# Optimization experiments

Hardware: AMD Instinct MI355X
Metric: run time of the kernel (lower is better)

The kernel has to match this reference:

```python
import jax, jax.numpy as jnp
import numpy as np

D_MODEL = 1024
NUM_HEADS = 16
HEAD_DIM = D_MODEL // NUM_HEADS
BATCH = 8
SEQ = 2048
LN_EPS = 1e-5


def setup_inputs() -> dict:
    rng = jax.random.key(0)
    ks = jax.random.split(rng, 16)
    s = 0.02  # init scale for weights
    w = lambda k: jax.random.normal(k, (D_MODEL, D_MODEL), jnp.float32) * s
    return {
        "query": jax.random.normal(ks[0], (BATCH, SEQ, D_MODEL), jnp.float32),
        "key": jax.random.normal(ks[1], (BATCH, SEQ, D_MODEL), jnp.float32),
        "value": jax.random.normal(ks[2], (BATCH, SEQ, D_MODEL), jnp.float32),
        "Wq": w(ks[3]), "bq": jnp.zeros((D_MODEL,), jnp.float32),
        "Wk": w(ks[4]), "bk": jnp.zeros((D_MODEL,), jnp.float32),
        "Wv": w(ks[5]), "bv": jnp.zeros((D_MODEL,), jnp.float32),
        "ln_g": jnp.ones((D_MODEL,), jnp.float32),
        "ln_b": jnp.zeros((D_MODEL,), jnp.float32),
        "Wo": w(ks[6]), "bo": jnp.zeros((D_MODEL,), jnp.float32),
    }


def reference(query, key, value, Wq, bq, Wk, bk, Wv, bv, ln_g, ln_b, Wo, bo):
    N, L, dm = query.shape
    H, Dh = NUM_HEADS, HEAD_DIM
    # projections + split heads -> (N, H, L, Dh), matching torch .view().transpose(1,2)
    q = (query @ Wq.T + bq).reshape(N, L, H, Dh).transpose(0, 2, 1, 3)
    k = (key   @ Wk.T + bk).reshape(N, L, H, Dh).transpose(0, 2, 1, 3)
    v = (value @ Wv.T + bv).reshape(N, L, H, Dh).transpose(0, 2, 1, 3)
    # Faithful to source: einsum 'nqhd,nkhd->nhqk' applied to ALREADY-transposed
    # (N,H,L,Dh) tensors => per-position head-to-head attention, energy (N, L, H, H).
    energy = jnp.einsum('nhld,ngld->nlhg', q, k)  # (N, L, H, H)
    attn = jax.nn.softmax(energy / jnp.sqrt(jnp.float32(dm)), axis=3)
    # source einsum 'nhql,nlhd->nqhd' on transposed v -> (N, H, L, Dh)
    out = jnp.einsum('nlhg,ngld->nhld', attn, v)
    out = out.transpose(0, 2, 1, 3).reshape(N, L, dm)
    # dropout is identity in eval mode
    mu = out.mean(axis=-1, keepdims=True)
    var = out.var(axis=-1, keepdims=True)
    out = (out - mu) / jnp.sqrt(var + LN_EPS) * ln_g + ln_b
    return out @ Wo.T + bo
```

## Files before the change

kernel.cpp:

```cpp
#include <hip/hip_runtime.h>
#include <cstdint>

#define TOKENS 16384
#define DMODEL 1024
#define NHEADS 16
#define HDIM   64

typedef __bf16  bf16x8 __attribute__((ext_vector_type(8)));
typedef ushort  u16x8  __attribute__((ext_vector_type(8)));
typedef ushort  u16x4  __attribute__((ext_vector_type(4)));
typedef short   s16x4  __attribute__((ext_vector_type(4)));
typedef float   f32x4  __attribute__((ext_vector_type(4)));

#if defined(__has_builtin)
#if __has_builtin(__builtin_amdgcn_mfma_f32_16x16x16bf16_1k)
#define HAVE_MFMA_K16 1
#endif
#endif

__device__ __forceinline__ ushort f2bf(float f) {
    union { float f; unsigned int i; } v; v.f = f;
    return (ushort)((v.i + 0x8000u) >> 16);
}
__device__ __forceinline__ f32x4 mfma16(bf16x8 a, bf16x8 b, f32x4 c) {
    return __builtin_amdgcn_mfma_f32_16x16x32_bf16(a, b, c, 0, 0, 0);
}
__device__ __forceinline__ void gload_lds16(const void* g, void* l) {
    __builtin_amdgcn_global_load_lds(
        (const __attribute__((address_space(1))) unsigned int*)(uintptr_t)g,
        (__attribute__((address_space(3))) unsigned int*)(uintptr_t)l,
        16, 0, 0);
}
union BU { u16x8 u; bf16x8 b; };

struct CvtArgs {
    const float* src[4];
    ushort*      dst[4];
};

__global__ __launch_bounds__(256) void cvt_f32_bf16(CvtArgs a)
{
    const float* __restrict__ s = a.src[blockIdx.y];
    ushort*      __restrict__ d = a.dst[blockIdx.y];
    const long i = ((long)blockIdx.x * 256 + threadIdx.x) * 8;
    const f32x4 v0 = *(const f32x4*)(s + i);
    const f32x4 v1 = *(const f32x4*)(s + i + 4);
    u16x8 p;
    #pragma unroll
    for (int j = 0; j < 4; j++) {
        p[j]     = f2bf(v0[j]);
        p[4 + j] = f2bf(v1[j]);
    }
    *(u16x8*)(d + i) = p;
}

#define BM2 256
#define BN2 256
#define BK2 32

struct GemmArgs {
    const ushort* A[3];
    const ushort* W[3];
    const float*  Bi[3];
    void*         C[3];
};

#define G256_READ_B(slot)                                                     \
    { _Pragma("unroll")                                                       \
      for (int n = 0; n < 4; ++n)                                             \
          bf[n] = *(const bf16x8*)&Bs[slot][(wn * 64 + n * 16 + fr) * BK2 + fks]; }

#define G256_READ_A(slot, mh)                                                 \
    { _Pragma("unroll")                                                       \
      for (int m = 0; m < 4; ++m)                                             \
          af[m] = *(const bf16x8*)&As[slot][(wm * 128 + (mh) * 64 + m * 16 + fr) * BK2 + fks]; }

#define G256_MFMA(mh)                                                         \
    { __builtin_amdgcn_s_setprio(1);                                          \
      _Pragma("unroll")                                                       \
      for (int m = 0; m < 4; ++m)                                             \
          _Pragma("unroll")                                                   \
          for (int n = 0; n < 4; ++n)                                         \
              acc[(mh) * 4 + m][n] = mfma16(af[m], bf[n], acc[(mh) * 4 + m][n]); \
      __builtin_amdgcn_s_setprio(0); }

template<int BF16OUT>
__global__ __launch_bounds__(512) void gemm256(GemmArgs args, int N, int K)
{
    __shared__ __align__(16) ushort As[4][BM2 * BK2];
    __shared__ __align__(16) ushort Bs[4][BN2 * BK2];

    const int gx = gridDim.x, gy = gridDim.y;
    const int lin = (blockIdx.z * gy + blockIdx.y) * gx + blockIdx.x;
    const int nwg = gx * gy * gridDim.z;
    const int q = nwg >> 3, r = nwg & 7;
    const int xcd = lin & 7, loc = lin >> 3;
    const int swz = (xcd < r ? xcd * (q + 1) : r * (q + 1) + (xcd - r) * q) + loc;
    const int bz  = swz / (gx * gy);
    const int rem = swz - bz * gx * gy;
    const int by  = rem / gx;
    const int bx  = rem - by * gx;

    const ushort* __restrict__ A  = args.A[bz];
    const ushort* __restrict__ W  = args.W[bz];
    const float*  __restrict__ Bi = args.Bi[bz];

    const int tid  = threadIdx.x;
    const int wave = tid >> 6;
    const int lane = tid & 63;
    const int wm = wave >> 2;
    const int wn = wave & 3;
    const long rowBase = (long)by * BM2;
    const long colBase = (long)bx * BN2;

    const int gA0 = tid, gA1 = tid + 512;
    const long aOff0 = (long)(gA0 >> 2) * K + (((gA0 & 3) ^ ((gA0 >> 3) & 3)) * 8);
    const long aOff1 = (long)(gA1 >> 2) * K + (((gA1 & 3) ^ ((gA1 >> 3) & 3)) * 8);
    const ushort* Abase = A + rowBase * K;
    const ushort* Wbase = W + colBase * K;

    const int fr  = lane & 15;
    const int fks = (((lane >> 4) ^ ((fr >> 1) & 3)) * 8);

    f32x4 acc[8][4];
    #pragma unroll
    for (int m = 0; m < 8; ++m)
        #pragma unroll
        for (int n = 0; n < 4; ++n)
            acc[m][n] = (f32x4){0.f, 0.f, 0.f, 0.f};

    auto stageA = [&](int slot, int kt) {
        gload_lds16(Abase + aOff0 + (long)kt * BK2, &As[slot][gA0 * 8]);
        gload_lds16(Abase + aOff1 + (long)kt * BK2, &As[slot][gA1 * 8]);
    };
    auto stageB = [&](int slot, int kt) {
        gload_lds16(Wbase + aOff0 + (long)kt * BK2, &Bs[slot][gA0 * 8]);
        gload_lds16(Wbase + aOff1 + (long)kt * BK2, &Bs[slot][gA1 * 8]);
    };

    const int nt = K / BK2;

    stageA(0, 0); stageB(0, 0);
    stageA(1, 1); stageB(1, 1);
    stageA(2, 2); stageB(2, 2);
    asm volatile("s_waitcnt vmcnt(8)" ::: "memory");
    __builtin_amdgcn_s_barrier();

    bf16x8 af[4], bf[4];

    for (int X = 0; X < nt - 3; ++X) {
        const int slot = X & 3, st = (X + 3) & 3;
        G256_READ_B(slot);
        G256_READ_A(slot, 0);
        stageA(st, X + 3);
        G256_MFMA(0);
        __builtin_amdgcn_s_barrier();
        G256_READ_A(slot, 1);
        stageB(st, X + 3);
        G256_MFMA(1);
        asm volatile("s_waitcnt vmcnt(8)" ::: "memory");
        __builtin_amdgcn_s_barrier();
    }
    {
        const int slot = (nt - 3) & 3;
        G256_READ_B(slot);
        G256_READ_A(slot, 0);
        G256_MFMA(0);
        __builtin_amdgcn_s_barrier();
        G256_READ_A(slot, 1);
        G256_MFMA(1);
        asm volatile("s_waitcnt vmcnt(4)" ::: "memory");
        __builtin_amdgcn_s_barrier();
    }
    {
        const int slot = (nt - 2) & 3;
        G256_READ_B(slot);
        G256_READ_A(slot, 0);
        G256_MFMA(0);
        __builtin_amdgcn_s_barrier();
        G256_READ_A(slot, 1);
        G256_MFMA(1);
        asm volatile("s_waitcnt vmcnt(0)" ::: "memory");
        __builtin_amdgcn_s_barrier();
    }
    {
        const int slot = (nt - 1) & 3;
        G256_READ_B(slot);
        G256_READ_A(slot, 0);
        G256_MFMA(0);
        __builtin_amdgcn_s_barrier();
        G256_READ_A(slot, 1);
        G256_MFMA(1);
    }

    const int qd = lane >> 4;
    #pragma unroll
    for (int n = 0; n < 4; ++n) {
        const long col = colBase + wn * 64 + n * 16 + fr;
        const float bv = Bi[col];
        #pragma unroll
        for (int m = 0; m < 8; ++m) {
            const long r0 = rowBase + wm * 128 + m * 16 + qd * 4;
            #pragma unroll
            for (int r2 = 0; r2 < 4; ++r2) {
                const float val = acc[m][n][r2] + bv;
                if (BF16OUT)
                    ((ushort*)args.C[bz])[(r0 + r2) * (long)N + col] = f2bf(val);
                else
                    ((float*)args.C[bz])[(r0 + r2) * (long)N + col] = val;
            }
        }
    }
}

#define PMS 40

__global__ __launch_bounds__(256) void attn_ln_mfma(
    const ushort* __restrict__ Qp, const ushort* __restrict__ Kp,
    const ushort* __restrict__ Vp,
    const float* __restrict__ lng, const float* __restrict__ lnb,
    ushort* __restrict__ O)
{
#if HAVE_MFMA_K16
    __shared__ __align__(16) ushort Vs[4][1024];
#else
    __shared__ __align__(16) ushort Vs[4][2048];
    __shared__ __align__(16) ushort Pm[4][16 * PMS];
#endif
    __shared__ __align__(16) float Os[4][16 * 68];

    const int tid  = threadIdx.x;
    const int w    = tid >> 6;
    const int lane = tid & 63;
    const long tok  = (long)blockIdx.x * 4 + w;
    const long base = tok * DMODEL;

    {
        const int i0 = lane, i1 = lane + 64;
        const int g0 = i0 >> 3, d80 = (i0 & 7) ^ (((i0 >> 5) & 3) << 1);
        const int g1 = i1 >> 3, d81 = (i1 & 7) ^ (((i1 >> 5) & 3) << 1);
        gload_lds16(Vp + base + g0 * 64 + d80 * 8, &Vs[w][i0 * 8]);
        gload_lds16(Vp + base + g1 * 64 + d81 * 8, &Vs[w][i1 * 8]);
    }

    const int fr = lane & 15;
    const int hi = lane >> 4;
    const int fs = hi * 8;

    const bf16x8 aq0 = *(const bf16x8*)(Qp + base + fr * 64 + fs);
    const bf16x8 aq1 = *(const bf16x8*)(Qp + base + fr * 64 + fs + 32);
    const bf16x8 bk0 = *(const bf16x8*)(Kp + base + fr * 64 + fs);
    const bf16x8 bk1 = *(const bf16x8*)(Kp + base + fr * 64 + fs + 32);

    f32x4 e = (f32x4){0.f, 0.f, 0.f, 0.f};
    e = mfma16(bk0, aq0, e);
    e = mfma16(bk1, aq1, e);

    float x[4];
    #pragma unroll
    for (int r = 0; r < 4; ++r) x[r] = e[r] * 0.03125f;
    float mx = fmaxf(fmaxf(x[0], x[1]), fmaxf(x[2], x[3]));
    mx = fmaxf(mx, __shfl_xor(mx, 16, 64));
    mx = fmaxf(mx, __shfl_xor(mx, 32, 64));
    float ex[4], sm;
    #pragma unroll
    for (int r = 0; r < 4; ++r) ex[r] = __expf(x[r] - mx);
    sm = (ex[0] + ex[1]) + (ex[2] + ex[3]);
    sm += __shfl_xor(sm, 16, 64);
    sm += __shfl_xor(sm, 32, 64);
    const float inv = 1.0f / sm;
    float p[4];
    #pragma unroll
    for (int r = 0; r < 4; ++r) p[r] = ex[r] * inv;

    f32x4 o[4];

#if HAVE_MFMA_K16
    s16x4 pa;
    #pragma unroll
    for (int r = 0; r < 4; ++r) pa[r] = (short)f2bf(p[r]);

    asm volatile("s_waitcnt vmcnt(0)" ::: "memory");

    #pragma unroll
    for (int dblk = 0; dblk < 4; ++dblk) {
        s16x4 bv;
        #pragma unroll
        for (int j = 0; j < 4; ++j) {
            const int g = hi * 4 + j;
            const int d = dblk * 16 + fr;
            const int ad = g * 64 + (((d >> 3) ^ (((g >> 2) & 3) << 1)) * 8) + (d & 7);
            bv[j] = (short)Vs[w][ad];
        }
        o[dblk] = __builtin_amdgcn_mfma_f32_16x16x16bf16_1k(
            pa, bv, (f32x4){0.f, 0.f, 0.f, 0.f}, 0, 0, 0);
    }
#else
    *(u16x4*)&Pm[w][fr * PMS + 16 + hi * 4] = (u16x4){0, 0, 0, 0};
    #pragma unroll
    for (int r = 0; r < 4; ++r)
        Pm[w][fr * PMS + hi * 4 + r] = f2bf(p[r]);
    asm volatile("s_waitcnt vmcnt(0)" ::: "memory");
    const bf16x8 pa8 = *(const bf16x8*)&Pm[w][fr * PMS + fs];
    #pragma unroll
    for (int dblk = 0; dblk < 4; ++dblk) {
        BU bu;
        #pragma unroll
        for (int j = 0; j < 8; ++j) {
            const int g = fs + j;
            const int d = dblk * 16 + fr;
            const int ad = g * 64 + (((d >> 3) ^ (((g >> 2) & 3) << 1)) * 8) + (d & 7);
            bu.u[j] = Vs[w][ad];
        }
        o[dblk] = mfma16(pa8, bu.b, (f32x4){0.f, 0.f, 0.f, 0.f});
    }
#endif

    float s1 = 0.f, s2 = 0.f;
    #pragma unroll
    for (int dblk = 0; dblk < 4; ++dblk)
        #pragma unroll
        for (int r = 0; r < 4; ++r) { const float v = o[dblk][r]; s1 += v; s2 += v * v; }
    #pragma unroll
    for (int m = 1; m < 64; m <<= 1) {
        s1 += __shfl_xor(s1, m, 64);
        s2 += __shfl_xor(s2, m, 64);
    }
    const float mu   = s1 * (1.f / DMODEL);
    const float var  = s2 * (1.f / DMODEL) - mu * mu;
    const float rstd = rsqrtf(var + 1e-5f);

    #pragma unroll
    for (int dblk = 0; dblk < 4; ++dblk)
        #pragma unroll
        for (int r = 0; r < 4; ++r)
            Os[w][(hi * 4 + r) * 68 + dblk * 16 + fr] = (o[dblk][r] - mu) * rstd;

    u16x8 s0, s1v;
    #pragma unroll
    for (int c = 0; c < 4; ++c) {
        const f32x4 yv = *(const f32x4*)&Os[w][(lane >> 2) * 68 + (lane & 3) * 16 + c * 4];
        const f32x4 lg = *(const f32x4*)(lng + lane * 16 + c * 4);
        const f32x4 lb = *(const f32x4*)(lnb + lane * 16 + c * 4);
        #pragma unroll
        for (int j = 0; j < 4; ++j) {
            const ushort hv = f2bf(yv[j] * lg[j] + lb[j]);
            if (c < 2) s0[c * 4 + j] = hv; else s1v[(c - 2) * 4 + j] = hv;
        }
    }
    *(u16x8*)(O + base + lane * 16)     = s0;
    *(u16x8*)(O + base + lane * 16 + 8) = s1v;
}

extern "C" void kernel_launch(void* const* d_in, const int* in_sizes, int n_in,
                              void* d_out, int out_size, void* d_ws, size_t ws_size,
                              hipStream_t stream)
{
    const float* query = (const float*)d_in[0];
    const float* key   = (const float*)d_in[1];
    const float* value = (const float*)d_in[2];
    const float* Wq = (const float*)d_in[3];
    const float* bq = (const float*)d_in[4];
    const float* Wk = (const float*)d_in[5];
    const float* bk = (const float*)d_in[6];
    const float* Wv = (const float*)d_in[7];
    const float* bv = (const float*)d_in[8];
    const float* lng = (const float*)d_in[9];
    const float* lnb = (const float*)d_in[10];
    const float* Wo = (const float*)d_in[11];
    const float* bo = (const float*)d_in[12];
    float* out = (float*)d_out;

    const long WELEMS = (long)DMODEL * DMODEL;

    ushort* wq_b = (ushort*)d_ws;
    ushort* wk_b = wq_b + WELEMS;
    ushort* wv_b = wk_b + WELEMS;
    ushort* wo_b = wv_b + WELEMS;
    ushort* cbuf = wo_b + WELEMS;

    int NC = 1;
    while (NC < 64 &&
           (size_t)(8 * WELEMS) + (size_t)(TOKENS / NC) * DMODEL * 10 > ws_size)
        NC <<= 1;
    const int CM = TOKENS / NC;
    const size_t CE = (size_t)CM * DMODEL;

    ushort* qb = cbuf;
    ushort* kb = qb + CE;
    ushort* vb = kb + CE;
    ushort* qp = vb + CE;
    ushort* vp = qp + CE;

    {
        CvtArgs cw;
        cw.src[0] = Wq; cw.src[1] = Wk; cw.src[2] = Wv; cw.src[3] = Wo;
        cw.dst[0] = wq_b; cw.dst[1] = wk_b; cw.dst[2] = wv_b; cw.dst[3] = wo_b;
        cvt_f32_bf16<<<dim3((unsigned)(WELEMS / 2048), 4), 256, 0, stream>>>(cw);
    }

    for (int c = 0; c < NC; ++c) {
        const size_t off = (size_t)c * CE;
        ushort* kp = (ushort*)(out + off);

        {
            CvtArgs ci;
            ci.src[0] = query + off; ci.src[1] = key + off; ci.src[2] = value + off;
            ci.src[3] = query;
            ci.dst[0] = qb; ci.dst[1] = kb; ci.dst[2] = vb; ci.dst[3] = qb;
            cvt_f32_bf16<<<dim3((unsigned)(CE / 2048), 3), 256, 0, stream>>>(ci);
        }

        GemmArgs g1;
        g1.A[0] = qb;    g1.A[1] = kb;   g1.A[2] = vb;
        g1.W[0] = wq_b;  g1.W[1] = wk_b; g1.W[2] = wv_b;
        g1.Bi[0] = bq;   g1.Bi[1] = bk;  g1.Bi[2] = bv;
        g1.C[0] = qp;    g1.C[1] = kp;   g1.C[2] = vp;
        gemm256<1><<<dim3(DMODEL / BN2, CM / BM2, 3), 512, 0, stream>>>(
            g1, DMODEL, DMODEL);

        attn_ln_mfma<<<CM / 4, 256, 0, stream>>>(qp, kp, vp, lng, lnb, qb);

        GemmArgs g2;
        g2.A[0] = g2.A[1] = g2.A[2] = qb;
        g2.W[0] = g2.W[1] = g2.W[2] = wo_b;
        g2.Bi[0] = g2.Bi[1] = g2.Bi[2] = bo;
        g2.C[0] = g2.C[1] = g2.C[2] = out + off;
        gemm256<0><<<dim3(DMODEL / BN2, CM / BM2, 1), 512, 0, stream>>>(
            g2, DMODEL, DMODEL);
    }
}
```

Measured before the change: 433.6 us.

## Fuse fp32-to-bf16 input conversion into QKV projection GEMM A-tile staging

The QKV GEMM now reads fp32 activations directly from global memory into registers, converts them to bf16 and writes them into swizzled LDS slots. A new register double-buffered pipeline replaces the async direct-to-LDS loads for A, which removes the separate conversion kernel and its bf16 round trip through memory. Attention now writes its output in place over the Q buffer, so the workspace needs fewer chunk buffers and fewer chunks may be used. The trade-offs are more register pressure, reading twice the A bytes inside the GEMM, and a more complex waitcnt schedule.

```diff
diff --git a/kernel.cpp b/kernel.cpp
--- a/kernel.cpp
+++ b/kernel.cpp
@@ -59,7 +59,7 @@
 #define BK2 32
 
 struct GemmArgs {
-    const ushort* A[3];
+    const void*   A[3];
     const ushort* W[3];
     const float*  Bi[3];
     void*         C[3];
@@ -84,7 +84,41 @@
               acc[(mh) * 4 + m][n] = mfma16(af[m], bf[n], acc[(mh) * 4 + m][n]); \
       __builtin_amdgcn_s_setprio(0); }
 
-template<int BF16OUT>
+#define ISSUE_A(P, kt)                                                        \
+    {   const float* ap_ = Af + (kt);                                         \
+        P##0 = *(const f32x4*)(ap_ + aF0);                                    \
+        P##1 = *(const f32x4*)(ap_ + aF0 + 4);                                \
+        P##2 = *(const f32x4*)(ap_ + aF1);                                    \
+        P##3 = *(const f32x4*)(ap_ + aF1 + 4);                                \
+    }
+#define WRITE_A(slot, P)                                                      \
+    {   u16x8 p0_, p1_;                                                       \
+        _Pragma("unroll")                                                     \
+        for (int j_ = 0; j_ < 4; ++j_) {                                      \
+            p0_[j_] = f2bf(P##0[j_]); p0_[4 + j_] = f2bf(P##1[j_]);           \
+            p1_[j_] = f2bf(P##2[j_]); p1_[4 + j_] = f2bf(P##3[j_]);           \
+        }                                                                     \
+        *(u16x8*)&As[slot][wg0 * 8] = p0_;                                    \
+        *(u16x8*)&As[slot][wg1 * 8] = p1_;                                    \
+    }
+
+#define STEADY_TILE(XV, IB, WB)                                               \
+    {   const int slot_ = (XV) & 3, st_ = ((XV) + 3) & 3;                     \
+        G256_READ_B(slot_);                                                   \
+        G256_READ_A(slot_, 0);                                                \
+        ISSUE_A(IB, ((XV) + 2) * BK2);                                        \
+        G256_MFMA(0);                                                         \
+        __builtin_amdgcn_s_barrier();                                         \
+        G256_READ_A(slot_, 1);                                                \
+        stageB(st_, (XV) + 3);                                                \
+        asm volatile("s_waitcnt vmcnt(8)" ::: "memory");                      \
+        WRITE_A(((XV) + 1) & 3, WB);                                          \
+        G256_MFMA(1);                                                         \
+        asm volatile("s_waitcnt lgkmcnt(0)" ::: "memory");                    \
+        __builtin_amdgcn_s_barrier();                                         \
+    }
+
+template<int BF16OUT, int AFP32>
 __global__ __launch_bounds__(512) void gemm256(GemmArgs args, int N, int K)
 {
     __shared__ __align__(16) ushort As[4][BM2 * BK2];
@@ -101,7 +135,6 @@
     const int by  = rem / gx;
     const int bx  = rem - by * gx;
 
-    const ushort* __restrict__ A  = args.A[bz];
     const ushort* __restrict__ W  = args.W[bz];
     const float*  __restrict__ Bi = args.Bi[bz];
 
@@ -114,10 +147,16 @@
     const long colBase = (long)bx * BN2;
 
     const int gA0 = tid, gA1 = tid + 512;
-    const long aOff0 = (long)(gA0 >> 2) * K + (((gA0 & 3) ^ ((gA0 >> 3) & 3)) * 8);
-    const long aOff1 = (long)(gA1 >> 2) * K + (((gA1 & 3) ^ ((gA1 >> 3) & 3)) * 8);
-    const ushort* Abase = A + rowBase * K;
+    const long sOff0 = (long)(gA0 >> 2) * K + (((gA0 & 3) ^ ((gA0 >> 3) & 3)) * 8);
+    const long sOff1 = (long)(gA1 >> 2) * K + (((gA1 & 3) ^ ((gA1 >> 3) & 3)) * 8);
     const ushort* Wbase = W + colBase * K;
+
+    const int arow0 = gA0 >> 2, arow1 = gA1 >> 2;
+    const long aF0 = (long)arow0 * K + (gA0 & 3) * 8;
+    const long aF1 = (long)arow1 * K + (gA1 & 3) * 8;
+    const int wg0 = arow0 * 4 + ((gA0 & 3) ^ ((arow0 >> 1) & 3));
+    const int wg1 = arow1 * 4 + ((gA1 & 3) ^ ((arow1 >> 1) & 3));
+    const float* Af = (const float*)args.A[bz] + rowBase * K;
 
     const int fr  = lane & 15;
     const int fks = (((lane >> 4) ^ ((fr >> 1) & 3)) * 8);
@@ -129,68 +168,126 @@
         for (int n = 0; n < 4; ++n)
             acc[m][n] = (f32x4){0.f, 0.f, 0.f, 0.f};
 
-    auto stageA = [&](int slot, int kt) {
-        gload_lds16(Abase + aOff0 + (long)kt * BK2, &As[slot][gA0 * 8]);
-        gload_lds16(Abase + aOff1 + (long)kt * BK2, &As[slot][gA1 * 8]);
+    auto stageB = [&](int slot, int kt) {
+        gload_lds16(Wbase + sOff0 + (long)kt * BK2, &Bs[slot][gA0 * 8]);
+        gload_lds16(Wbase + sOff1 + (long)kt * BK2, &Bs[slot][gA1 * 8]);
     };
-    auto stageB = [&](int slot, int kt) {
-        gload_lds16(Wbase + aOff0 + (long)kt * BK2, &Bs[slot][gA0 * 8]);
-        gload_lds16(Wbase + aOff1 + (long)kt * BK2, &Bs[slot][gA1 * 8]);
-    };
 
     const int nt = K / BK2;
-
-    stageA(0, 0); stageB(0, 0);
-    stageA(1, 1); stageB(1, 1);
-    stageA(2, 2); stageB(2, 2);
-    asm volatile("s_waitcnt vmcnt(8)" ::: "memory");
-    __builtin_amdgcn_s_barrier();
-
     bf16x8 af[4], bf[4];
 
-    for (int X = 0; X < nt - 3; ++X) {
-        const int slot = X & 3, st = (X + 3) & 3;
-        G256_READ_B(slot);
-        G256_READ_A(slot, 0);
-        stageA(st, X + 3);
-        G256_MFMA(0);
+    if constexpr (AFP32) {
+        f32x4 arA0, arA1, arA2, arA3, arB0, arB1, arB2, arB3;
+
+        ISSUE_A(arA, 0);
+        ISSUE_A(arB, BK2);
+        stageB(0, 0); stageB(1, 1); stageB(2, 2);
+        asm volatile("s_waitcnt vmcnt(10)" ::: "memory");
+        WRITE_A(0, arA);
+        asm volatile("s_waitcnt vmcnt(4)" ::: "memory");
+        asm volatile("s_waitcnt lgkmcnt(0)" ::: "memory");
         __builtin_amdgcn_s_barrier();
-        G256_READ_A(slot, 1);
-        stageB(st, X + 3);
-        G256_MFMA(1);
+
+        int X = 0;
+        for (; X + 1 <= nt - 5; X += 2) {
+            STEADY_TILE(X,     arA, arB);
+            STEADY_TILE(X + 1, arB, arA);
+        }
+        STEADY_TILE(nt - 4, arA, arB);
+
+        {
+            const int slot_ = (nt - 3) & 3;
+            G256_READ_B(slot_);
+            G256_READ_A(slot_, 0);
+            ISSUE_A(arB, (nt - 1) * BK2);
+            G256_MFMA(0);
+            __builtin_amdgcn_s_barrier();
+            G256_READ_A(slot_, 1);
+            asm volatile("s_waitcnt vmcnt(6)" ::: "memory");
+            WRITE_A((nt - 2) & 3, arA);
+            G256_MFMA(1);
+            asm volatile("s_waitcnt lgkmcnt(0)" ::: "memory");
+            __builtin_amdgcn_s_barrier();
+        }
+        {
+            const int slot_ = (nt - 2) & 3;
+            G256_READ_B(slot_);
+            G256_READ_A(slot_, 0);
+            G256_MFMA(0);
+            __builtin_amdgcn_s_barrier();
+            G256_READ_A(slot_, 1);
+            asm volatile("s_waitcnt vmcnt(0)" ::: "memory");
+            WRITE_A((nt - 1) & 3, arB);
+            G256_MFMA(1);
+            asm volatile("s_waitcnt lgkmcnt(0)" ::: "memory");
+            __builtin_amdgcn_s_barrier();
+        }
+        {
+            const int slot_ = (nt - 1) & 3;
+            G256_READ_B(slot_);
+            G256_READ_A(slot_, 0);
+            G256_MFMA(0);
+            __builtin_amdgcn_s_barrier();
+            G256_READ_A(slot_, 1);
+            G256_MFMA(1);
+        }
+    } else {
+        const ushort* Abase = (const ushort*)args.A[bz] + rowBase * K;
+        auto stageA = [&](int slot, int kt) {
+            gload_lds16(Abase + sOff0 + (long)kt * BK2, &As[slot][gA0 * 8]);
+            gload_lds16(Abase + sOff1 + (long)kt * BK2, &As[slot][gA1 * 8]);
+        };
+
+        stageA(0, 0); stageB(0, 0);
+        stageA(1, 1); stageB(1, 1);
+        stageA(2, 2); stageB(2, 2);
         asm volatile("s_waitcnt vmcnt(8)" ::: "memory");
         __builtin_amdgcn_s_barrier();
-    }
-    {
-        const int slot = (nt - 3) & 3;
-        G256_READ_B(slot);
-        G256_READ_A(slot, 0);
-        G256_MFMA(0);
-        __builtin_amdgcn_s_barrier();
-        G256_READ_A(slot, 1);
-        G256_MFMA(1);
-        asm volatile("s_waitcnt vmcnt(4)" ::: "memory");
-        __builtin_amdgcn_s_barrier();
-    }
-    {
-        const int slot = (nt - 2) & 3;
-        G256_READ_B(slot);
-        G256_READ_A(slot, 0);
-        G256_MFMA(0);
-        __builtin_amdgcn_s_barrier();
-        G256_READ_A(slot, 1);
-        G256_MFMA(1);
-        asm volatile("s_waitcnt vmcnt(0)" ::: "memory");
-        __builtin_amdgcn_s_barrier();
-    }
-    {
-        const int slot = (nt - 1) & 3;
-        G256_READ_B(slot);
-        G256_READ_A(slot, 0);
-        G256_MFMA(0);
-        __builtin_amdgcn_s_barrier();
-        G256_READ_A(slot, 1);
-        G256_MFMA(1);
+
+        for (int X = 0; X < nt - 3; ++X) {
+            const int slot_ = X & 3, st_ = (X + 3) & 3;
+            G256_READ_B(slot_);
+            G256_READ_A(slot_, 0);
+            stageA(st_, X + 3);
+            G256_MFMA(0);
+            __builtin_amdgcn_s_barrier();
+            G256_READ_A(slot_, 1);
+            stageB(st_, X + 3);
+            G256_MFMA(1);
+            asm volatile("s_waitcnt vmcnt(8)" ::: "memory");
+            __builtin_amdgcn_s_barrier();
+        }
+        {
+            const int slot_ = (nt - 3) & 3;
+            G256_READ_B(slot_);
+            G256_READ_A(slot_, 0);
+            G256_MFMA(0);
+            __builtin_amdgcn_s_barrier();
+            G256_READ_A(slot_, 1);
+            G256_MFMA(1);
+            asm volatile("s_waitcnt vmcnt(4)" ::: "memory");
+            __builtin_amdgcn_s_barrier();
+        }
+        {
+            const int slot_ = (nt - 2) & 3;
+            G256_READ_B(slot_);
+            G256_READ_A(slot_, 0);
+            G256_MFMA(0);
+            __builtin_amdgcn_s_barrier();
+            G256_READ_A(slot_, 1);
+            G256_MFMA(1);
+            asm volatile("s_waitcnt vmcnt(0)" ::: "memory");
+            __builtin_amdgcn_s_barrier();
+        }
+        {
+            const int slot_ = (nt - 1) & 3;
+            G256_READ_B(slot_);
+            G256_READ_A(slot_, 0);
+            G256_MFMA(0);
+            __builtin_amdgcn_s_barrier();
+            G256_READ_A(slot_, 1);
+            G256_MFMA(1);
+        }
     }
 
     const int qd = lane >> 4;
@@ -216,10 +313,10 @@
 #define PMS 40
 
 __global__ __launch_bounds__(256) void attn_ln_mfma(
-    const ushort* __restrict__ Qp, const ushort* __restrict__ Kp,
+    const ushort* Qp, const ushort* __restrict__ Kp,
     const ushort* __restrict__ Vp,
     const float* __restrict__ lng, const float* __restrict__ lnb,
-    ushort* __restrict__ O)
+    ushort* O)
 {
 #if HAVE_MFMA_K16
     __shared__ __align__(16) ushort Vs[4][1024];
@@ -381,15 +478,12 @@
 
     int NC = 1;
     while (NC < 64 &&
-           (size_t)(8 * WELEMS) + (size_t)(TOKENS / NC) * DMODEL * 10 > ws_size)
+           (size_t)(8 * WELEMS) + (size_t)(TOKENS / NC) * DMODEL * 4 > ws_size)
         NC <<= 1;
     const int CM = TOKENS / NC;
     const size_t CE = (size_t)CM * DMODEL;
 
-    ushort* qb = cbuf;
-    ushort* kb = qb + CE;
-    ushort* vb = kb + CE;
-    ushort* qp = vb + CE;
+    ushort* qp = cbuf;
     ushort* vp = qp + CE;
 
     {
@@ -403,30 +497,22 @@
         const size_t off = (size_t)c * CE;
         ushort* kp = (ushort*)(out + off);
 
-        {
-            CvtArgs ci;
-            ci.src[0] = query + off; ci.src[1] = key + off; ci.src[2] = value + off;
-            ci.src[3] = query;
-            ci.dst[0] = qb; ci.dst[1] = kb; ci.dst[2] = vb; ci.dst[3] = qb;
-            cvt_f32_bf16<<<dim3((unsigned)(CE / 2048), 3), 256, 0, stream>>>(ci);
-        }
-
         GemmArgs g1;
-        g1.A[0] = qb;    g1.A[1] = kb;   g1.A[2] = vb;
+        g1.A[0] = query + off; g1.A[1] = key + off; g1.A[2] = value + off;
         g1.W[0] = wq_b;  g1.W[1] = wk_b; g1.W[2] = wv_b;
         g1.Bi[0] = bq;   g1.Bi[1] = bk;  g1.Bi[2] = bv;
         g1.C[0] = qp;    g1.C[1] = kp;   g1.C[2] = vp;
-        gemm256<1><<<dim3(DMODEL / BN2, CM / BM2, 3), 512, 0, stream>>>(
+        gemm256<1, 1><<<dim3(DMODEL / BN2, CM / BM2, 3), 512, 0, stream>>>(
             g1, DMODEL, DMODEL);
 
-        attn_ln_mfma<<<CM / 4, 256, 0, stream>>>(qp, kp, vp, lng, lnb, qb);
+        attn_ln_mfma<<<CM / 4, 256, 0, stream>>>(qp, kp, vp, lng, lnb, qp);
 
         GemmArgs g2;
-        g2.A[0] = g2.A[1] = g2.A[2] = qb;
+        g2.A[0] = g2.A[1] = g2.A[2] = qp;
         g2.W[0] = g2.W[1] = g2.W[2] = wo_b;
         g2.Bi[0] = g2.Bi[1] = g2.Bi[2] = bo;
         g2.C[0] = g2.C[1] = g2.C[2] = out + off;
-        gemm256<0><<<dim3(DMODEL / BN2, CM / BM2, 1), 512, 0, stream>>>(
+        gemm256<0, 0><<<dim3(DMODEL / BN2, CM / BM2, 1), 512, 0, stream>>>(
             g2, DMODEL, DMODEL);
     }
 }
```

Result: faster. 393.5 us (-9.2%).
